# Kernel tuning notes

Hardware: AMD Instinct MI355X
Metric: run time of the kernel (lower is better)

## Reference

```python
import jax, jax.numpy as jnp
import numpy as np

M, N, H, C = 50000, 50000, 32, 128
K, GROUPS = 15, 8
CPG = C // GROUPS           # 16, channels per group
RADIUS, SIGMA, INF = 2.5, 1.0, 1.0e6
EPS = 1e-5                  # GroupNorm eps
NEG_SLOPE = 0.1             # LeakyReLU slope in alpha MLP


def setup_inputs() -> dict:
    key = jax.random.key(0)
    ks = jax.random.split(key, 12)
    q_pts = jax.random.normal(ks[0], (M, 3), jnp.float32) * 5.0
    s_pts = q_pts  # same-resolution layer: q == s
    s_feats = jax.random.normal(ks[1], (N, C), jnp.float32)
    neighb_inds = jax.random.randint(ks[2], (M, H), 0, N + 1)  # N = padding index
    # kernel points: center + 14 points in a sphere of given radius
    kp = jax.random.normal(ks[3], (K, 3), jnp.float32)
    kp = kp / (jnp.linalg.norm(kp, axis=1, keepdims=True) + 1e-9) * RADIUS * 0.66
    k_pts = kp.at[0].set(0.0)
    # alpha MLP: Linear(C->C) + LeakyReLU + Linear(C->K*CPG)
    W1 = jax.random.normal(ks[4], (C, C), jnp.float32) * np.sqrt(2.0 / C)
    b1 = jnp.zeros((C,), jnp.float32)
    W2 = jax.random.normal(ks[5], (C, K * CPG), jnp.float32) * np.sqrt(2.0 / C)
    b2 = jnp.zeros((K * CPG,), jnp.float32)
    gn_w = jnp.ones((K * CPG,), jnp.float32)
    gn_b = jnp.zeros((K * CPG,), jnp.float32)
    return {"q_pts": q_pts, "s_pts": s_pts, "s_feats": s_feats,
            "neighb_inds": neighb_inds, "k_pts": k_pts,
            "W1": W1, "b1": b1, "W2": W2, "b2": b2,
            "gn_w": gn_w, "gn_b": gn_b}


def reference(q_pts, s_pts, s_feats, k_pts, W1, b1, W2, b2, gn_w, gn_b, neighb_inds):
    m = q_pts.shape[0]
    # ---- neighbor geometry (no_grad in original) ----
    s_pts_pad = jnp.concatenate([s_pts, jnp.full((1, 3), INF, s_pts.dtype)], 0)
    neighbors = s_pts_pad[neighb_inds] - q_pts[:, None, :]          # (M,H,3)
    sq = jnp.sum((neighbors[:, :, None, :] - k_pts) ** 2, -1)       # (M,H,K)
    nn_sq = jnp.min(sq, -1)                                         # (M,H)
    nn_1nn = jnp.argmin(sq, -1)                                     # (M,H)
    infl = jnp.clip(1.0 - jnp.sqrt(nn_sq) / SIGMA, 0.0)             # linear influence
    # ---- neighbor features gather (padding row = zeros) ----
    feats_pad = jnp.concatenate([s_feats, jnp.zeros((1, C), s_feats.dtype)], 0)
    neighbor_feats = feats_pad[neighb_inds]                         # (M,H,C)
    # ---- dynamic weights from center features (q==s -> pooled = s_feats) ----
    pooled = s_feats
    h = pooled @ W1 + b1
    h = jnp.where(h >= 0, h, NEG_SLOPE * h)                         # LeakyReLU(0.1)
    cw = (h @ W2 + b2).reshape(m, K, CPG)                           # (M,K,CPG)
    # GroupNorm(K groups over K*CPG channels), stats over (points, CPG) per group
    mu = jnp.mean(cw, axis=(0, 2), keepdims=True)
    var = jnp.var(cw, axis=(0, 2), keepdims=True)
    cw = (cw - mu) * jax.lax.rsqrt(var + EPS)
    cw = cw * gn_w.reshape(1, K, CPG) + gn_b.reshape(1, K, CPG)
    # ---- gather weights at nearest kernel point, modulate by influence ----
    nw = jnp.take_along_axis(cw, nn_1nn[:, :, None], axis=1)        # (M,H,CPG)
    nw = nw * infl[:, :, None]                                      # weight_act = identity
    # ---- multiply and sum over neighbors ----
    nf = neighbor_feats.reshape(m, H, CPG, GROUPS)
    out = jnp.sum(nf * nw[:, :, :, None], axis=1)                   # (M,CPG,GROUPS)
    return out.reshape(m, C)
```

## Files before the change

kernel.cpp:

```cpp
#include <hip/hip_runtime.h>
#include <hip/hip_bf16.h>

#define Mpts 50000
#define Npts 50000
#define Hn 32
#define Cc 128
#define Kk 15
#define NCW 240

typedef __attribute__((ext_vector_type(8))) short short8;
typedef __attribute__((ext_vector_type(4))) float f32x4;
typedef __attribute__((ext_vector_type(2))) float f32x2;
typedef unsigned int u32;

__device__ inline ushort f2bf(float f) {
  __hip_bfloat16 h = __float2bfloat16(f);
  return *reinterpret_cast<ushort*>(&h);
}

__global__ __launch_bounds__(256) void k0_pre(
    const float* __restrict__ sfeat, const float* __restrict__ W1,
    const float* __restrict__ W2, ushort* __restrict__ sfb,
    ushort* __restrict__ W1t, ushort* __restrict__ W2t,
    float* __restrict__ stats)
{
  __shared__ ushort TT[240][66];
  const int t = threadIdx.x;
  const int b = blockIdx.x;
  if (b < 3125) {
    const size_t base = ((size_t)b * 256 + t) * 8;
    float4 f0 = *(const float4*)(sfeat + base);
    float4 f1 = *(const float4*)(sfeat + base + 4);
    union { short8 v; ushort u[8]; } pk;
    pk.u[0] = f2bf(f0.x); pk.u[1] = f2bf(f0.y); pk.u[2] = f2bf(f0.z); pk.u[3] = f2bf(f0.w);
    pk.u[4] = f2bf(f1.x); pk.u[5] = f2bf(f1.y); pk.u[6] = f2bf(f1.z); pk.u[7] = f2bf(f1.w);
    *(short8*)(sfb + base) = pk.v;
  } else if (b < 3127) {
    const int k0 = (b - 3125) * 64;
#pragma unroll
    for (int i = 0; i < 32; ++i) {
      int e = t + i * 256;
      int r = e >> 7, c = e & 127;
      TT[c][r] = f2bf(W1[(size_t)(k0 + r) * Cc + c]);
    }
    __syncthreads();
    int n = t >> 1, half = t & 1;
    union { short8 v[4]; ushort u[32]; } pk;
#pragma unroll
    for (int i = 0; i < 32; ++i) pk.u[i] = TT[n][half * 32 + i];
#pragma unroll
    for (int q = 0; q < 4; ++q)
      *(short8*)(W1t + (size_t)n * Cc + k0 + half * 32 + q * 8) = pk.v[q];
  } else if (b < 3129) {
    const int k0 = (b - 3127) * 64;
    for (int i = 0; i < 60; ++i) {
      int e = t + i * 256;
      int r = e / 240, c = e % 240;
      TT[c][r] = f2bf(W2[(size_t)(k0 + r) * NCW + c]);
    }
    __syncthreads();
    if (t < 240) {
      union { short8 v[8]; ushort u[64]; } pk;
#pragma unroll
      for (int i = 0; i < 64; ++i) pk.u[i] = TT[t][i];
#pragma unroll
      for (int q = 0; q < 8; ++q)
        *(short8*)(W2t + (size_t)t * Cc + k0 + q * 8) = pk.v[q];
    }
  } else {
    if (t < 16) {
      short8 z = short8{0,0,0,0,0,0,0,0};
      *(short8*)(sfb + (size_t)Npts * Cc + t * 8) = z;
    }
    if (t < 128) {
      float4 z4 = make_float4(0.f, 0.f, 0.f, 0.f);
      *(float4*)(stats + t * 4) = z4;
    }
  }
}

__global__ __launch_bounds__(256, 3) void k1_mlp(
    const ushort* __restrict__ sfb, const ushort* __restrict__ W1t,
    const float* __restrict__ b1, const ushort* __restrict__ W2t,
    const float* __restrict__ b2, ushort* __restrict__ cw,
    float* __restrict__ stats)
{
  __shared__ __align__(16) ushort shA[64 * 128];
  __shared__ __align__(16) ushort shW[128 * 128];
  __shared__ float red[2][15][4];

  const int t = threadIdx.x;
  const int r0 = blockIdx.x * 64;
  const int wid = t >> 6, lane = t & 63;
  const int l16 = lane & 15, lq = lane >> 4;

  uint4 av[4];
#pragma unroll
  for (int p = 0; p < 4; ++p) {
    int id = p * 256 + t;
    int r = id >> 4, c = id & 15;
    int g = r0 + r; if (g > Mpts) g = Mpts;
    av[p] = *(const uint4*)(sfb + (size_t)g * Cc + c * 8);
  }
  uint4 wv[8];
#pragma unroll
  for (int p = 0; p < 8; ++p) {
    int id = p * 256 + t;
    int r = id >> 4, c = id & 15;
    wv[p] = *(const uint4*)(W1t + r * Cc + c * 8);
  }
  asm volatile("" :: "v"(wv[0].x), "v"(wv[1].x), "v"(wv[2].x), "v"(wv[3].x),
                     "v"(wv[4].x), "v"(wv[5].x), "v"(wv[6].x), "v"(wv[7].x),
                     "v"(av[0].x), "v"(av[1].x), "v"(av[2].x), "v"(av[3].x));
#pragma unroll
  for (int p = 0; p < 8; ++p) {
    int id = p * 256 + t;
    int r = id >> 4, c = id & 15;
    *(uint4*)((char*)shW + ((r * 256 + c * 16) ^ ((r & 7) << 4))) = wv[p];
  }
#pragma unroll
  for (int p = 0; p < 4; ++p) {
    int id = p * 256 + t;
    int r = id >> 4, c = id & 15;
    *(uint4*)((char*)shA + ((r * 256 + c * 16) ^ ((r & 7) << 4))) = av[p];
  }
  __syncthreads();

  const int arow = wid * 16 + l16;
  const int axor = (arow & 7) << 4;

  f32x4 acc1[8];
#pragma unroll
  for (int nt = 0; nt < 8; ++nt) acc1[nt] = f32x4{0.f, 0.f, 0.f, 0.f};
#pragma unroll
  for (int kt = 0; kt < 4; ++kt) {
    const int koff2 = (kt * 32 + lq * 8) * 2;
    short8 a = *(const short8*)((const char*)shA + ((arow * 256 + koff2) ^ axor));
#pragma unroll
    for (int nt = 0; nt < 8; ++nt) {
      int wrow = nt * 16 + l16;
      short8 b = *(const short8*)((const char*)shW + ((wrow * 256 + koff2) ^ ((wrow & 7) << 4)));
      acc1[nt] = __builtin_amdgcn_mfma_f32_16x16x32_bf16(a, b, acc1[nt], 0, 0, 0);
    }
  }
#pragma unroll
  for (int nt = 0; nt < 8; ++nt) {
    int col = nt * 16 + l16;
    float bias = b1[col];
#pragma unroll
    for (int reg = 0; reg < 4; ++reg) {
      float h = acc1[nt][reg] + bias;
      h = h >= 0.f ? h : 0.1f * h;
      int row = wid * 16 + lq * 4 + reg;
      int byte = ((row * 256) + col * 2) ^ ((row & 7) << 4);
      *(ushort*)((char*)shA + byte) = f2bf(h);
    }
  }

  f32x4 acc2[8], acc3[7];
#pragma unroll
  for (int j = 0; j < 8; ++j) acc2[j] = f32x4{0.f, 0.f, 0.f, 0.f};
#pragma unroll
  for (int j = 0; j < 7; ++j) acc3[j] = f32x4{0.f, 0.f, 0.f, 0.f};

  __syncthreads();
  {
    uint4 wv2[8];
#pragma unroll
    for (int p = 0; p < 8; ++p) {
      int id = p * 256 + t;
      int r = id >> 4, c = id & 15;
      wv2[p] = *(const uint4*)(W2t + (size_t)r * Cc + c * 8);
    }
    asm volatile("" :: "v"(wv2[0].x), "v"(wv2[1].x), "v"(wv2[2].x), "v"(wv2[3].x),
                       "v"(wv2[4].x), "v"(wv2[5].x), "v"(wv2[6].x), "v"(wv2[7].x));
#pragma unroll
    for (int p = 0; p < 8; ++p) {
      int id = p * 256 + t;
      int r = id >> 4, c = id & 15;
      *(uint4*)((char*)shW + ((r * 256 + c * 16) ^ ((r & 7) << 4))) = wv2[p];
    }
  }
  __syncthreads();
#pragma unroll
  for (int kt = 0; kt < 4; ++kt) {
    const int koff2 = (kt * 32 + lq * 8) * 2;
    short8 a = *(const short8*)((const char*)shA + ((arow * 256 + koff2) ^ axor));
#pragma unroll
    for (int j = 0; j < 8; ++j) {
      int wrow = j * 16 + l16;
      short8 b = *(const short8*)((const char*)shW + ((wrow * 256 + koff2) ^ ((wrow & 7) << 4)));
      acc2[j] = __builtin_amdgcn_mfma_f32_16x16x32_bf16(a, b, acc2[j], 0, 0, 0);
    }
  }

  __syncthreads();
  {
    uint4 wv2[7];
#pragma unroll
    for (int p = 0; p < 7; ++p) {
      int id = p * 256 + t;
      int r = id >> 4, c = id & 15;
      wv2[p] = *(const uint4*)(W2t + (size_t)(128 + r) * Cc + c * 8);
    }
    asm volatile("" :: "v"(wv2[0].x), "v"(wv2[1].x), "v"(wv2[2].x), "v"(wv2[3].x),
                       "v"(wv2[4].x), "v"(wv2[5].x), "v"(wv2[6].x));
#pragma unroll
    for (int p = 0; p < 7; ++p) {
      int id = p * 256 + t;
      int r = id >> 4, c = id & 15;
      *(uint4*)((char*)shW + ((r * 256 + c * 16) ^ ((r & 7) << 4))) = wv2[p];
    }
  }
  __syncthreads();
#pragma unroll
  for (int kt = 0; kt < 4; ++kt) {
    const int koff2 = (kt * 32 + lq * 8) * 2;
    short8 a = *(const short8*)((const char*)shA + ((arow * 256 + koff2) ^ axor));
#pragma unroll
    for (int j = 0; j < 7; ++j) {
      int wrow = j * 16 + l16;
      short8 b = *(const short8*)((const char*)shW + ((wrow * 256 + koff2) ^ ((wrow & 7) << 4)));
      acc3[j] = __builtin_amdgcn_mfma_f32_16x16x32_bf16(a, b, acc3[j], 0, 0, 0);
    }
  }
  __syncthreads();

  ushort* shB = shW;
  float s[15], ss[15];
#pragma unroll
  for (int j = 0; j < 15; ++j) { s[j] = 0.f; ss[j] = 0.f; }
  const int rowb = wid * 16 + lq * 4;
#pragma unroll
  for (int j = 0; j < 15; ++j) {
    int col = j * 16 + l16;
    float bias = b2[col];
#pragma unroll
    for (int reg = 0; reg < 4; ++reg) {
      float v = (j < 8 ? acc2[j][reg] : acc3[j - 8][reg]) + bias;
      shB[(rowb + reg) * 244 + col] = f2bf(v);
      if (r0 + rowb + reg < Mpts) { s[j] += v; ss[j] += v * v; }
    }
  }
  __syncthreads();

  {
    char* cwB = (char*)cw + (size_t)r0 * 480;
#pragma unroll
    for (int i = 0; i < 8; ++i) {
      int gid = i * 256 + t;
      if (gid < 1920) {
        int row = gid / 30;
        int rem = (gid - row * 30) * 16;
        if (r0 + row < Mpts) {
          uint4 v = *(const uint4*)((const char*)shB + row * 488 + rem);
          *(uint4*)(cwB + (size_t)row * 480 + rem) = v;
        }
      }
    }
  }

#pragma unroll
  for (int j = 0; j < 15; ++j) {
    for (int off = 32; off > 0; off >>= 1) {
      s[j]  += __shfl_xor(s[j],  off);
      ss[j] += __shfl_xor(ss[j], off);
    }
  }
  if (lane == 0) {
#pragma unroll
    for (int j = 0; j < 15; ++j) { red[0][j][wid] = s[j]; red[1][j][wid] = ss[j]; }
  }
  __syncthreads();
  float* st = stats + (blockIdx.x & 7) * 64;
  if (t < 15) {
    float S = red[0][t][0] + red[0][t][1] + red[0][t][2] + red[0][t][3];
    atomicAdd(&st[t], S);
  } else if (t >= 32 && t < 47) {
    int j = t - 32;
    float SS = red[1][j][0] + red[1][j][1] + red[1][j][2] + red[1][j][3];
    atomicAdd(&st[32 + j], SS);
  }
}

__global__ __launch_bounds__(256) void k2_geom(
    const float* __restrict__ q_pts, const float* __restrict__ s_pts,
    const int* __restrict__ nb, const float* __restrict__ kp,
    const float* __restrict__ gn_w, const float* __restrict__ gn_b,
    const float* __restrict__ stats, u32* __restrict__ geomP,
    float* __restrict__ AtabG, float* __restrict__ BtabG)
{
  __shared__ float kpt[3][15];
  __shared__ float mus[16], rss[16];
  const int t = threadIdx.x;
  if (t < 45) kpt[t % 3][t / 3] = kp[t];
  __syncthreads();

  const int gtid = blockIdx.x * 256 + t;
  const int m = gtid >> 5;
  int idx = nb[gtid]; if (idx > Npts) idx = Npts;
  float qx = q_pts[m * 3 + 0], qy = q_pts[m * 3 + 1], qz = q_pts[m * 3 + 2];
  float px, py, pz;
  if (idx < Npts) { px = s_pts[idx * 3 + 0]; py = s_pts[idx * 3 + 1]; pz = s_pts[idx * 3 + 2]; }
  else            { px = 1.0e6f; py = 1.0e6f; pz = 1.0e6f; }
  float nx = px - qx, ny = py - qy, nz = pz - qz;
  int ksel = 0; float best = 1e30f;
#pragma unroll
  for (int k = 0; k < Kk; ++k) {
    float dx = nx - kpt[0][k], dy = ny - kpt[1][k], dz = nz - kpt[2][k];
    float d = dx * dx + dy * dy + dz * dz;
    if (d < best) { best = d; ksel = k; }
  }
  float infl = 1.f - sqrtf(best);
  infl = infl > 0.f ? infl : 0.f;
  geomP[gtid] = (__float_as_uint(infl) & 0xFFFFFFF0u) | (u32)ksel;

  if (blockIdx.x == 0) {
    if (t < 15) {
      float S = 0.f, SS = 0.f;
#pragma unroll
      for (int r = 0; r < 8; ++r) { S += stats[r * 64 + t]; SS += stats[r * 64 + 32 + t]; }
      const float inv = 1.0f / (16.0f * (float)Mpts);
      float mu = S * inv;
      float var = SS * inv - mu * mu;
      mus[t] = mu;
      rss[t] = rsqrtf(var + 1e-5f);
    }
    __syncthreads();
    if (t < 240) {
      int g = t >> 4;
      float a = rss[g] * gn_w[t];
      AtabG[t] = a;
      BtabG[t] = gn_b[t] - mus[g] * a;
    }
  }
}

__global__ __launch_bounds__(256) void k3_out(
    const ushort* __restrict__ sfb, const int* __restrict__ nb,
    const u32* __restrict__ geomP, const float* __restrict__ AtabG,
    const float* __restrict__ BtabG, const ushort* __restrict__ cw,
    float* __restrict__ out)
{
  __shared__ float Atab[255], Btab[255];
  __shared__ float wtab[4][2][8][33];
  const int t = threadIdx.x;
  if (t < 240) {
    int k = t >> 4, c = t & 15;
    Atab[k * 17 + c] = AtabG[t];
    Btab[k * 17 + c] = BtabG[t];
  }
  __syncthreads();

  const int half = (blockIdx.x >= 6250) ? 1 : 0;
  const int pblk = blockIdx.x - half * 6250;
  const int wid = t >> 6, lane = t & 63;
  const int mbase = pblk * 8 + wid * 2;
  const int gtid = pblk * 256 + t;
  const int ch = lane & 7, hlane = (lane >> 3) & 3, p = lane >> 5;
  const int half8 = half * 8;

  u32 g = geomP[gtid];
  int idxv = nb[gtid]; if (idxv > Npts) idxv = Npts;

  const uint4* fb = (const uint4*)sfb;
  uint4 fv[8];
#pragma unroll
  for (int j = 0; j < 8; ++j) {
    int ih = __shfl(idxv, (p << 5) | (hlane + 4 * j));
    fv[j] = fb[ih * 16 + half8 + ch];
  }

  {
    int h = lane >> 1, c0 = (lane & 1) * 4;
#pragma unroll
    for (int q = 0; q < 2; ++q) {
      u32 gp = __shfl((int)g, (q << 5) | h);
      int kh = gp & 15;
      float wI = __uint_as_float(gp & 0xFFFFFFF0u);
      uint2 cwv = *(const uint2*)(cw + (size_t)(mbase + q) * NCW + kh * 16 + half8 + c0);
      const float* Ar = &Atab[kh * 17 + half8 + c0];
      const float* Br = &Btab[kh * 17 + half8 + c0];
      float v0 = __uint_as_float(cwv.x << 16);
      float v1 = __uint_as_float(cwv.x & 0xffff0000u);
      float v2 = __uint_as_float(cwv.y << 16);
      float v3 = __uint_as_float(cwv.y & 0xffff0000u);
      wtab[wid][q][c0 + 0][h] = fmaf(v0, Ar[0], Br[0]) * wI;
      wtab[wid][q][c0 + 1][h] = fmaf(v1, Ar[1], Br[1]) * wI;
      wtab[wid][q][c0 + 2][h] = fmaf(v2, Ar[2], Br[2]) * wI;
      wtab[wid][q][c0 + 3][h] = fmaf(v3, Ar[3], Br[3]) * wI;
    }
  }

  asm volatile("" :: "v"(fv[0].x), "v"(fv[1].x), "v"(fv[2].x), "v"(fv[3].x),
                     "v"(fv[4].x), "v"(fv[5].x), "v"(fv[6].x), "v"(fv[7].x));

  f32x2 a0 = {0.f, 0.f}, a1 = {0.f, 0.f}, a2 = {0.f, 0.f}, a3 = {0.f, 0.f};
#pragma unroll
  for (int j = 0; j < 8; ++j) {
    float w = wtab[wid][p][ch][hlane + 4 * j];
    f32x2 w2 = {w, w};
    u32 ux = fv[j].x, uy = fv[j].y, uz = fv[j].z, uw = fv[j].w;
    f32x2 q0 = {__uint_as_float(ux << 16), __uint_as_float(ux & 0xffff0000u)};
    f32x2 q1 = {__uint_as_float(uy << 16), __uint_as_float(uy & 0xffff0000u)};
    f32x2 q2 = {__uint_as_float(uz << 16), __uint_as_float(uz & 0xffff0000u)};
    f32x2 q3 = {__uint_as_float(uw << 16), __uint_as_float(uw & 0xffff0000u)};
    a0 = __builtin_elementwise_fma(q0, w2, a0);
    a1 = __builtin_elementwise_fma(q1, w2, a1);
    a2 = __builtin_elementwise_fma(q2, w2, a2);
    a3 = __builtin_elementwise_fma(q3, w2, a3);
  }
#pragma unroll
  for (int off = 8; off <= 16; off <<= 1) {
    a0[0] += __shfl_xor(a0[0], off); a0[1] += __shfl_xor(a0[1], off);
    a1[0] += __shfl_xor(a1[0], off); a1[1] += __shfl_xor(a1[1], off);
    a2[0] += __shfl_xor(a2[0], off); a2[1] += __shfl_xor(a2[1], off);
    a3[0] += __shfl_xor(a3[0], off); a3[1] += __shfl_xor(a3[1], off);
  }
  if ((lane & 24) == 0) {
    float* op = out + (size_t)(mbase + p) * Cc + half * 64 + ch * 8;
    float4 o0; o0.x = a0[0]; o0.y = a0[1]; o0.z = a1[0]; o0.w = a1[1];
    float4 o1; o1.x = a2[0]; o1.y = a2[1]; o1.z = a3[0]; o1.w = a3[1];
    *(float4*)(op)     = o0;
    *(float4*)(op + 4) = o1;
  }
}

extern "C" void kernel_launch(void* const* d_in, const int* in_sizes, int n_in,
                              void* d_out, int out_size, void* d_ws, size_t ws_size,
                              hipStream_t stream) {
  const float* q_pts  = (const float*)d_in[0];
  const float* s_pts  = (const float*)d_in[1];
  const float* sfeat  = (const float*)d_in[2];
  const int*   nb     = (const int*)d_in[3];
  const float* kp     = (const float*)d_in[4];
  const float* W1     = (const float*)d_in[5];
  const float* b1     = (const float*)d_in[6];
  const float* W2     = (const float*)d_in[7];
  const float* b2     = (const float*)d_in[8];
  const float* gn_w   = (const float*)d_in[9];
  const float* gn_b   = (const float*)d_in[10];
  float* out   = (float*)d_out;

  char* wsb = (char*)d_ws;
  float*  stats = (float*)wsb;
  ushort* sfb   = (ushort*)(wsb + 4096);
  ushort* W1t   = (ushort*)(wsb + 12804352);
  ushort* W2t   = (ushort*)(wsb + 12837120);
  ushort* cwb   = (ushort*)(wsb + 12898560);
  u32*    geomP = (u32*)   (wsb + 36898560);
  float*  AtabG = (float*) (wsb + 43298560);
  float*  BtabG = (float*) (wsb + 43299520);

  k0_pre <<<3130, 256, 0, stream>>>(sfeat, W1, W2, sfb, W1t, W2t, stats);
  k1_mlp <<<(Mpts + 63) / 64, 256, 0, stream>>>(sfb, W1t, b1, W2t, b2, cwb, stats);
  k2_geom<<<6250, 256, 0, stream>>>(q_pts, s_pts, nb, kp, gn_w, gn_b, stats,
                                    geomP, AtabG, BtabG);
  k3_out <<<12500, 256, 0, stream>>>(sfb, nb, geomP, AtabG, BtabG, cwb, out);
}
```

Measured before the change: 104.6 us.

## Fuse geometry into prep kernel, bf16 conversion into MLP, quarter-split output

```diff
diff --git a/kernel.cpp b/kernel.cpp
--- a/kernel.cpp
+++ b/kernel.cpp
@@ -19,24 +19,40 @@
 }
 
 __global__ __launch_bounds__(256) void k0_pre(
-    const float* __restrict__ sfeat, const float* __restrict__ W1,
-    const float* __restrict__ W2, ushort* __restrict__ sfb,
-    ushort* __restrict__ W1t, ushort* __restrict__ W2t,
-    float* __restrict__ stats)
+    const float* __restrict__ q_pts, const float* __restrict__ s_pts,
+    const int* __restrict__ nb, const float* __restrict__ kp,
+    const float* __restrict__ W1, const float* __restrict__ W2,
+    ushort* __restrict__ sfb, ushort* __restrict__ W1t,
+    ushort* __restrict__ W2t, float* __restrict__ stats,
+    u32* __restrict__ geomP)
 {
-  __shared__ ushort TT[240][66];
   const int t = threadIdx.x;
   const int b = blockIdx.x;
-  if (b < 3125) {
-    const size_t base = ((size_t)b * 256 + t) * 8;
-    float4 f0 = *(const float4*)(sfeat + base);
-    float4 f1 = *(const float4*)(sfeat + base + 4);
-    union { short8 v; ushort u[8]; } pk;
-    pk.u[0] = f2bf(f0.x); pk.u[1] = f2bf(f0.y); pk.u[2] = f2bf(f0.z); pk.u[3] = f2bf(f0.w);
-    pk.u[4] = f2bf(f1.x); pk.u[5] = f2bf(f1.y); pk.u[6] = f2bf(f1.z); pk.u[7] = f2bf(f1.w);
-    *(short8*)(sfb + base) = pk.v;
-  } else if (b < 3127) {
-    const int k0 = (b - 3125) * 64;
+  if (b < 6250) {
+    __shared__ float kpt[3][15];
+    if (t < 45) kpt[t % 3][t / 3] = kp[t];
+    __syncthreads();
+    const int gtid = b * 256 + t;
+    const int m = gtid >> 5;
+    int idx = nb[gtid]; if (idx > Npts) idx = Npts;
+    float qx = q_pts[m * 3 + 0], qy = q_pts[m * 3 + 1], qz = q_pts[m * 3 + 2];
+    float px, py, pz;
+    if (idx < Npts) { px = s_pts[idx * 3 + 0]; py = s_pts[idx * 3 + 1]; pz = s_pts[idx * 3 + 2]; }
+    else            { px = 1.0e6f; py = 1.0e6f; pz = 1.0e6f; }
+    float nx = px - qx, ny = py - qy, nz = pz - qz;
+    int ksel = 0; float best = 1e30f;
+#pragma unroll
+    for (int k = 0; k < Kk; ++k) {
+      float dx = nx - kpt[0][k], dy = ny - kpt[1][k], dz = nz - kpt[2][k];
+      float d = dx * dx + dy * dy + dz * dz;
+      if (d < best) { best = d; ksel = k; }
+    }
+    float infl = 1.f - sqrtf(best);
+    infl = infl > 0.f ? infl : 0.f;
+    geomP[gtid] = (__float_as_uint(infl) & 0xFFFFFFF0u) | (u32)ksel;
+  } else if (b < 6252) {
+    __shared__ ushort TT[240][66];
+    const int k0 = (b - 6250) * 64;
 #pragma unroll
     for (int i = 0; i < 32; ++i) {
       int e = t + i * 256;
@@ -51,8 +67,9 @@
 #pragma unroll
     for (int q = 0; q < 4; ++q)
       *(short8*)(W1t + (size_t)n * Cc + k0 + half * 32 + q * 8) = pk.v[q];
-  } else if (b < 3129) {
-    const int k0 = (b - 3127) * 64;
+  } else if (b < 6254) {
+    __shared__ ushort TT[240][66];
+    const int k0 = (b - 6252) * 64;
     for (int i = 0; i < 60; ++i) {
       int e = t + i * 256;
       int r = e / 240, c = e % 240;
@@ -80,10 +97,10 @@
 }
 
 __global__ __launch_bounds__(256, 3) void k1_mlp(
-    const ushort* __restrict__ sfb, const ushort* __restrict__ W1t,
+    const float* __restrict__ sfeat, const ushort* __restrict__ W1t,
     const float* __restrict__ b1, const ushort* __restrict__ W2t,
-    const float* __restrict__ b2, ushort* __restrict__ cw,
-    float* __restrict__ stats)
+    const float* __restrict__ b2, ushort* __restrict__ sfb,
+    ushort* __restrict__ cw, float* __restrict__ stats)
 {
   __shared__ __align__(16) ushort shA[64 * 128];
   __shared__ __align__(16) ushort shW[128 * 128];
@@ -94,13 +111,19 @@
   const int wid = t >> 6, lane = t & 63;
   const int l16 = lane & 15, lq = lane >> 4;
 
-  uint4 av[4];
+  float4 fA[4], fB[4];
 #pragma unroll
   for (int p = 0; p < 4; ++p) {
     int id = p * 256 + t;
     int r = id >> 4, c = id & 15;
-    int g = r0 + r; if (g > Mpts) g = Mpts;
-    av[p] = *(const uint4*)(sfb + (size_t)g * Cc + c * 8);
+    int g = r0 + r;
+    fA[p] = make_float4(0.f, 0.f, 0.f, 0.f);
+    fB[p] = make_float4(0.f, 0.f, 0.f, 0.f);
+    if (g < Mpts) {
+      const float* src = sfeat + (size_t)g * Cc + c * 8;
+      fA[p] = *(const float4*)(src);
+      fB[p] = *(const float4*)(src + 4);
+    }
   }
   uint4 wv[8];
 #pragma unroll
@@ -111,7 +134,8 @@
   }
   asm volatile("" :: "v"(wv[0].x), "v"(wv[1].x), "v"(wv[2].x), "v"(wv[3].x),
                      "v"(wv[4].x), "v"(wv[5].x), "v"(wv[6].x), "v"(wv[7].x),
-                     "v"(av[0].x), "v"(av[1].x), "v"(av[2].x), "v"(av[3].x));
+                     "v"(fA[0].x), "v"(fA[1].x), "v"(fA[2].x), "v"(fA[3].x),
+                     "v"(fB[0].x), "v"(fB[1].x), "v"(fB[2].x), "v"(fB[3].x));
 #pragma unroll
   for (int p = 0; p < 8; ++p) {
     int id = p * 256 + t;
@@ -122,7 +146,12 @@
   for (int p = 0; p < 4; ++p) {
     int id = p * 256 + t;
     int r = id >> 4, c = id & 15;
-    *(uint4*)((char*)shA + ((r * 256 + c * 16) ^ ((r & 7) << 4))) = av[p];
+    int g = r0 + r;
+    union { short8 s; ushort u[8]; } pk;
+    pk.u[0] = f2bf(fA[p].x); pk.u[1] = f2bf(fA[p].y); pk.u[2] = f2bf(fA[p].z); pk.u[3] = f2bf(fA[p].w);
+    pk.u[4] = f2bf(fB[p].x); pk.u[5] = f2bf(fB[p].y); pk.u[6] = f2bf(fB[p].z); pk.u[7] = f2bf(fB[p].w);
+    if (g < Mpts) *(short8*)(sfb + (size_t)g * Cc + c * 8) = pk.s;
+    *(short8*)((char*)shA + ((r * 256 + c * 16) ^ ((r & 7) << 4))) = pk.s;
   }
   __syncthreads();
 
@@ -283,122 +312,79 @@
   }
 }
 
-__global__ __launch_bounds__(256) void k2_geom(
-    const float* __restrict__ q_pts, const float* __restrict__ s_pts,
-    const int* __restrict__ nb, const float* __restrict__ kp,
-    const float* __restrict__ gn_w, const float* __restrict__ gn_b,
-    const float* __restrict__ stats, u32* __restrict__ geomP,
-    float* __restrict__ AtabG, float* __restrict__ BtabG)
-{
-  __shared__ float kpt[3][15];
-  __shared__ float mus[16], rss[16];
-  const int t = threadIdx.x;
-  if (t < 45) kpt[t % 3][t / 3] = kp[t];
-  __syncthreads();
-
-  const int gtid = blockIdx.x * 256 + t;
-  const int m = gtid >> 5;
-  int idx = nb[gtid]; if (idx > Npts) idx = Npts;
-  float qx = q_pts[m * 3 + 0], qy = q_pts[m * 3 + 1], qz = q_pts[m * 3 + 2];
-  float px, py, pz;
-  if (idx < Npts) { px = s_pts[idx * 3 + 0]; py = s_pts[idx * 3 + 1]; pz = s_pts[idx * 3 + 2]; }
-  else            { px = 1.0e6f; py = 1.0e6f; pz = 1.0e6f; }
-  float nx = px - qx, ny = py - qy, nz = pz - qz;
-  int ksel = 0; float best = 1e30f;
-#pragma unroll
-  for (int k = 0; k < Kk; ++k) {
-    float dx = nx - kpt[0][k], dy = ny - kpt[1][k], dz = nz - kpt[2][k];
-    float d = dx * dx + dy * dy + dz * dz;
-    if (d < best) { best = d; ksel = k; }
-  }
-  float infl = 1.f - sqrtf(best);
-  infl = infl > 0.f ? infl : 0.f;
-  geomP[gtid] = (__float_as_uint(infl) & 0xFFFFFFF0u) | (u32)ksel;
-
-  if (blockIdx.x == 0) {
-    if (t < 15) {
-      float S = 0.f, SS = 0.f;
-#pragma unroll
-      for (int r = 0; r < 8; ++r) { S += stats[r * 64 + t]; SS += stats[r * 64 + 32 + t]; }
-      const float inv = 1.0f / (16.0f * (float)Mpts);
-      float mu = S * inv;
-      float var = SS * inv - mu * mu;
-      mus[t] = mu;
-      rss[t] = rsqrtf(var + 1e-5f);
-    }
-    __syncthreads();
-    if (t < 240) {
-      int g = t >> 4;
-      float a = rss[g] * gn_w[t];
-      AtabG[t] = a;
-      BtabG[t] = gn_b[t] - mus[g] * a;
-    }
-  }
-}
-
 __global__ __launch_bounds__(256) void k3_out(
     const ushort* __restrict__ sfb, const int* __restrict__ nb,
-    const u32* __restrict__ geomP, const float* __restrict__ AtabG,
-    const float* __restrict__ BtabG, const ushort* __restrict__ cw,
-    float* __restrict__ out)
+    const u32* __restrict__ geomP, const float* __restrict__ gn_w,
+    const float* __restrict__ gn_b, const float* __restrict__ stats,
+    const ushort* __restrict__ cw, float* __restrict__ out)
 {
   __shared__ float Atab[255], Btab[255];
-  __shared__ float wtab[4][2][8][33];
+  __shared__ float mus[16], rss[16];
+  __shared__ float wtab[4][2][32][6];
   const int t = threadIdx.x;
+
+  if (t < 15) {
+    float S = 0.f, SS = 0.f;
+#pragma unroll
+    for (int r = 0; r < 8; ++r) { S += stats[r * 64 + t]; SS += stats[r * 64 + 32 + t]; }
+    const float inv = 1.0f / (16.0f * (float)Mpts);
+    float mu = S * inv;
+    float var = SS * inv - mu * mu;
+    mus[t] = mu;
+    rss[t] = rsqrtf(var + 1e-5f);
+  }
+  __syncthreads();
   if (t < 240) {
     int k = t >> 4, c = t & 15;
-    Atab[k * 17 + c] = AtabG[t];
-    Btab[k * 17 + c] = BtabG[t];
-  }
-  __syncthreads();
-
-  const int half = (blockIdx.x >= 6250) ? 1 : 0;
-  const int pblk = blockIdx.x - half * 6250;
+    float a = rss[k] * gn_w[t];
+    Atab[k * 17 + c] = a;
+    Btab[k * 17 + c] = gn_b[t] - mus[k] * a;
+  }
+  __syncthreads();
+
+  const int quarter = blockIdx.x / 6250;
+  const int pblk = blockIdx.x - quarter * 6250;
   const int wid = t >> 6, lane = t & 63;
   const int mbase = pblk * 8 + wid * 2;
   const int gtid = pblk * 256 + t;
-  const int ch = lane & 7, hlane = (lane >> 3) & 3, p = lane >> 5;
-  const int half8 = half * 8;
+  const int ch = lane & 3, hlane = (lane >> 2) & 7, p = lane >> 5;
+  const int q4 = quarter * 4;
 
   u32 g = geomP[gtid];
   int idxv = nb[gtid]; if (idxv > Npts) idxv = Npts;
 
   const uint4* fb = (const uint4*)sfb;
-  uint4 fv[8];
-#pragma unroll
-  for (int j = 0; j < 8; ++j) {
-    int ih = __shfl(idxv, (p << 5) | (hlane + 4 * j));
-    fv[j] = fb[ih * 16 + half8 + ch];
+  uint4 fv[4];
+#pragma unroll
+  for (int j = 0; j < 4; ++j) {
+    int ih = __shfl(idxv, (p << 5) | (hlane + 8 * j));
+    fv[j] = fb[ih * 16 + q4 + ch];
   }
 
   {
-    int h = lane >> 1, c0 = (lane & 1) * 4;
+    int h = lane >> 1, c0 = (lane & 1) * 2;
 #pragma unroll
     for (int q = 0; q < 2; ++q) {
       u32 gp = __shfl((int)g, (q << 5) | h);
       int kh = gp & 15;
       float wI = __uint_as_float(gp & 0xFFFFFFF0u);
-      uint2 cwv = *(const uint2*)(cw + (size_t)(mbase + q) * NCW + kh * 16 + half8 + c0);
-      const float* Ar = &Atab[kh * 17 + half8 + c0];
-      const float* Br = &Btab[kh * 17 + half8 + c0];
-      float v0 = __uint_as_float(cwv.x << 16);
-      float v1 = __uint_as_float(cwv.x & 0xffff0000u);
-      float v2 = __uint_as_float(cwv.y << 16);
-      float v3 = __uint_as_float(cwv.y & 0xffff0000u);
-      wtab[wid][q][c0 + 0][h] = fmaf(v0, Ar[0], Br[0]) * wI;
-      wtab[wid][q][c0 + 1][h] = fmaf(v1, Ar[1], Br[1]) * wI;
-      wtab[wid][q][c0 + 2][h] = fmaf(v2, Ar[2], Br[2]) * wI;
-      wtab[wid][q][c0 + 3][h] = fmaf(v3, Ar[3], Br[3]) * wI;
-    }
-  }
-
-  asm volatile("" :: "v"(fv[0].x), "v"(fv[1].x), "v"(fv[2].x), "v"(fv[3].x),
-                     "v"(fv[4].x), "v"(fv[5].x), "v"(fv[6].x), "v"(fv[7].x));
+      u32 cwv = *(const u32*)(cw + (size_t)(mbase + q) * NCW + kh * 16 + q4 + c0);
+      int jj = kh * 17 + q4 + c0;
+      float v0 = __uint_as_float(cwv << 16);
+      float v1 = __uint_as_float(cwv & 0xffff0000u);
+      f32x2 w2;
+      w2[0] = fmaf(v0, Atab[jj],     Btab[jj])     * wI;
+      w2[1] = fmaf(v1, Atab[jj + 1], Btab[jj + 1]) * wI;
+      *(f32x2*)&wtab[wid][q][h][c0] = w2;
+    }
+  }
+
+  asm volatile("" :: "v"(fv[0].x), "v"(fv[1].x), "v"(fv[2].x), "v"(fv[3].x));
 
   f32x2 a0 = {0.f, 0.f}, a1 = {0.f, 0.f}, a2 = {0.f, 0.f}, a3 = {0.f, 0.f};
 #pragma unroll
-  for (int j = 0; j < 8; ++j) {
-    float w = wtab[wid][p][ch][hlane + 4 * j];
+  for (int j = 0; j < 4; ++j) {
+    float w = wtab[wid][p][hlane + 8 * j][ch];
     f32x2 w2 = {w, w};
     u32 ux = fv[j].x, uy = fv[j].y, uz = fv[j].z, uw = fv[j].w;
     f32x2 q0 = {__uint_as_float(ux << 16), __uint_as_float(ux & 0xffff0000u)};
@@ -411,14 +397,14 @@
     a3 = __builtin_elementwise_fma(q3, w2, a3);
   }
 #pragma unroll
-  for (int off = 8; off <= 16; off <<= 1) {
+  for (int off = 4; off <= 16; off <<= 1) {
     a0[0] += __shfl_xor(a0[0], off); a0[1] += __shfl_xor(a0[1], off);
     a1[0] += __shfl_xor(a1[0], off); a1[1] += __shfl_xor(a1[1], off);
     a2[0] += __shfl_xor(a2[0], off); a2[1] += __shfl_xor(a2[1], off);
     a3[0] += __shfl_xor(a3[0], off); a3[1] += __shfl_xor(a3[1], off);
   }
-  if ((lane & 24) == 0) {
-    float* op = out + (size_t)(mbase + p) * Cc + half * 64 + ch * 8;
+  if ((lane & 28) == 0) {
+    float* op = out + (size_t)(mbase + p) * Cc + quarter * 32 + ch * 8;
     float4 o0; o0.x = a0[0]; o0.y = a0[1]; o0.z = a1[0]; o0.w = a1[1];
     float4 o1; o1.x = a2[0]; o1.y = a2[1]; o1.z = a3[0]; o1.w = a3[1];
     *(float4*)(op)     = o0;
@@ -449,12 +435,11 @@
   ushort* W2t   = (ushort*)(wsb + 12837120);
   ushort* cwb   = (ushort*)(wsb + 12898560);
   u32*    geomP = (u32*)   (wsb + 36898560);
-  float*  AtabG = (float*) (wsb + 43298560);
-  float*  BtabG = (float*) (wsb + 43299520);
-
-  k0_pre <<<3130, 256, 0, stream>>>(sfeat, W1, W2, sfb, W1t, W2t, stats);
-  k1_mlp <<<(Mpts + 63) / 64, 256, 0, stream>>>(sfb, W1t, b1, W2t, b2, cwb, stats);
-  k2_geom<<<6250, 256, 0, stream>>>(q_pts, s_pts, nb, kp, gn_w, gn_b, stats,
-                                    geomP, AtabG, BtabG);
-  k3_out <<<12500, 256, 0, stream>>>(sfb, nb, geomP, AtabG, BtabG, cwb, out);
+
+  k0_pre<<<6255, 256, 0, stream>>>(q_pts, s_pts, nb, kp, W1, W2,
+                                   sfb, W1t, W2t, stats, geomP);
+  k1_mlp<<<(Mpts + 63) / 64, 256, 0, stream>>>(sfeat, W1t, b1, W2t, b2,
+                                               sfb, cwb, stats);
+  k3_out<<<25000, 256, 0, stream>>>(sfb, nb, geomP, gn_w, gn_b, stats,
+                                    cwb, out);
 }
```

Result: slower. 144.0 us (+37.7%).
